# Kernel tuning notes

Hardware: AMD Instinct MI355X
Metric: run time of the kernel (lower is better)

Reference implementation:

```python
import jax, jax.numpy as jnp
import numpy as np

LN_EPS = 1e-5
LEAKY_SLOPE = 0.01  # torch nn.LeakyReLU default negative_slope


def layer_norm(x, gamma, beta):
    mu = jnp.mean(x, axis=-1, keepdims=True)
    var = jnp.mean(jnp.square(x - mu), axis=-1, keepdims=True)
    return (x - mu) * jax.lax.rsqrt(var + LN_EPS) * gamma + beta


def setup_inputs() -> dict:
    key = jax.random.key(0)
    k1, k2, k3 = jax.random.split(key, 3)
    B, N, D = 32, 128, 64
    embeddings = jax.random.normal(k1, (B, N, D), dtype=jnp.float32)
    ln_gamma = jnp.ones((D,), dtype=jnp.float32)
    ln_beta = jnp.zeros((D,), dtype=jnp.float32)
    # nn.Linear(3*D, 1): weight [1, 3D], bias [1]
    bound = 1.0 / np.sqrt(3 * D)
    att_w = jax.random.uniform(k2, (1, 3 * D), dtype=jnp.float32, minval=-bound, maxval=bound)
    att_b = jax.random.uniform(k3, (1,), dtype=jnp.float32, minval=-bound, maxval=bound)
    return {"embeddings": embeddings, "ln_gamma": ln_gamma, "ln_beta": ln_beta,
            "att_w": att_w, "att_b": att_b}


def reference(embeddings, ln_gamma, ln_beta, att_w, att_b):
    # embeddings: [B, N, D]
    D = embeddings.shape[-1]
    w = att_w[0]
    w_q, w_k, w_v = w[:D], w[D:2 * D], w[2 * D:]

    # value = query * key (all-pairs elementwise product), [B, N, N, D]
    value = embeddings[:, :, None, :] * embeddings[:, None, :, :]

    # LayerNorm of the broadcast query/key is just a per-node LayerNorm,
    # broadcast N-fold -> compute once per node, then contract with the
    # corresponding slice of the concat-linear weight.
    ln_e = layer_norm(embeddings, ln_gamma, ln_beta)           # [B, N, D]
    q_score = ln_e @ w_q                                        # [B, N]
    k_score = ln_e @ w_k                                        # [B, N]
    v_score = jnp.einsum('bijd,d->bij', layer_norm(value, ln_gamma, ln_beta), w_v)

    # score = Linear(concat(wq, wk, wv)) : [B, N, N]
    score = q_score[:, :, None] + k_score[:, None, :] + v_score + att_b[0]
    score = jnp.where(score >= 0, score, LEAKY_SLOPE * score)   # LeakyReLU
    # dropout is identity in eval mode
    alphas = jax.nn.softmax(score, axis=-1)[..., None]          # [B, N, N, 1]
    return (alphas, value)
```

## Files before the change

### kernel.cpp

```cpp
#include <hip/hip_runtime.h>

#define N_TOK 128
#define DIM   64
#define LN_EPS 1e-5f
#define SLOPE  0.01f

__device__ __forceinline__ float wave_reduce_sum(float v) {
#pragma unroll
    for (int off = 32; off >= 1; off >>= 1) v += __shfl_xor(v, off, 64);
    return v;
}
__device__ __forceinline__ float wave_reduce_max(float v) {
#pragma unroll
    for (int off = 32; off >= 1; off >>= 1) v = fmaxf(v, __shfl_xor(v, off, 64));
    return v;
}

__global__ __launch_bounds__(256) void k0_row_stats(
        const float* __restrict__ emb, const float* __restrict__ gamma,
        const float* __restrict__ beta, const float* __restrict__ attw,
        float* __restrict__ q_ws, float* __restrict__ k_ws, int nrows) {
    int wave = threadIdx.x >> 6, lane = threadIdx.x & 63;
    int r = blockIdx.x * 4 + wave;
    if (r >= nrows) return;
    float e  = emb[r * DIM + lane];
    float g  = gamma[lane], bt = beta[lane];
    float wq = attw[lane], wk = attw[DIM + lane];
    float gwq = g * wq, gwk = g * wk;

    float se  = wave_reduce_sum(e);
    float se2 = wave_reduce_sum(e * e);
    float sq  = wave_reduce_sum(e * gwq);
    float sk  = wave_reduce_sum(e * gwk);
    float Sgq = wave_reduce_sum(gwq);
    float Sbq = wave_reduce_sum(bt * wq);
    float Sgk = wave_reduce_sum(gwk);
    float Sbk = wave_reduce_sum(bt * wk);

    if (lane == 0) {
        float mu  = se * (1.f / 64.f);
        float var = se2 * (1.f / 64.f) - mu * mu;
        float rsq = rsqrtf(var + LN_EPS);
        q_ws[r] = rsq * (sq - mu * Sgq) + Sbq;
        k_ws[r] = rsq * (sk - mu * Sgk) + Sbk;
    }
}

__global__ __launch_bounds__(256) void k12_fused(
        const float* __restrict__ emb, const float* __restrict__ gamma,
        const float* __restrict__ beta, const float* __restrict__ attw,
        const float* __restrict__ attb, const float* __restrict__ q_ws,
        const float* __restrict__ k_ws, float* __restrict__ alphas,
        float4* __restrict__ value4) {
    __shared__ float sc_lds[N_TOK];

    int b = blockIdx.x >> 7;
    int i = blockIdx.x & 127;
    int c  = threadIdx.x & 15;
    int jg = threadIdx.x >> 4;

    const float4* E4 = (const float4*)emb + ((size_t)(b * N_TOK) << 4);
    float4 a4  = E4[(i << 4) | c];
    float4 g4  = ((const float4*)gamma)[c];
    float4 bt4 = ((const float4*)beta)[c];
    float4 wv4 = ((const float4*)(attw + 2 * DIM))[c];
    float gwx = g4.x * wv4.x, gwy = g4.y * wv4.y,
          gwz = g4.z * wv4.z, gww = g4.w * wv4.w;

    float Sg = gwx + gwy + gwz + gww;
    float Sb = bt4.x * wv4.x + bt4.y * wv4.y + bt4.z * wv4.z + bt4.w * wv4.w;
#pragma unroll
    for (int off = 1; off < 16; off <<= 1) {
        Sg += __shfl_xor(Sg, off);
        Sb += __shfl_xor(Sb, off);
    }
    float qi = q_ws[b * N_TOK + i] + attb[0];

    float4* vrow = value4 + ((size_t)blockIdx.x << 11);

#pragma unroll
    for (int it = 0; it < 8; ++it) {
        int j = (it << 4) | jg;
        float4 e4 = E4[(j << 4) | c];
        float4 t4;
        t4.x = a4.x * e4.x; t4.y = a4.y * e4.y;
        t4.z = a4.z * e4.z; t4.w = a4.w * e4.w;
        vrow[(j << 4) | c] = t4;

        float s1 = t4.x + t4.y + t4.z + t4.w;
        float s2 = t4.x * t4.x + t4.y * t4.y + t4.z * t4.z + t4.w * t4.w;
        float s3 = t4.x * gwx + t4.y * gwy + t4.z * gwz + t4.w * gww;
#pragma unroll
        for (int off = 1; off < 16; off <<= 1) {
            s1 += __shfl_xor(s1, off);
            s2 += __shfl_xor(s2, off);
            s3 += __shfl_xor(s3, off);
        }
        if (c == 0) {
            float mu  = s1 * (1.f / 64.f);
            float var = s2 * (1.f / 64.f) - mu * mu;
            float rsq = rsqrtf(var + LN_EPS);
            float vsc = rsq * (s3 - mu * Sg) + Sb;
            float sc  = qi + k_ws[b * N_TOK + j] + vsc;
            sc_lds[j] = sc >= 0.f ? sc : SLOPE * sc;
        }
    }
    __syncthreads();

    if (threadIdx.x < 64) {
        int lane = threadIdx.x;
        float va = sc_lds[lane];
        float vb = sc_lds[lane + 64];
        float m  = wave_reduce_max(fmaxf(va, vb));
        float ea = __expf(va - m), eb = __expf(vb - m);
        float s  = wave_reduce_sum(ea + eb);
        float inv = 1.f / s;
        float* arow = alphas + ((size_t)blockIdx.x << 7);
        arow[lane]      = ea * inv;
        arow[lane + 64] = eb * inv;
    }
}

extern "C" void kernel_launch(void* const* d_in, const int* in_sizes, int n_in,
                              void* d_out, int out_size, void* d_ws, size_t ws_size,
                              hipStream_t stream) {
    const float* emb   = (const float*)d_in[0];
    const float* gamma = (const float*)d_in[1];
    const float* beta  = (const float*)d_in[2];
    const float* attw  = (const float*)d_in[3];
    const float* attb  = (const float*)d_in[4];
    float* out = (float*)d_out;

    int B = in_sizes[0] / (N_TOK * DIM);
    int nrows = B * N_TOK;
    float* q_ws = (float*)d_ws;
    float* k_ws = q_ws + nrows;

    float* alphas = out;
    float* value  = out + (size_t)nrows * N_TOK;

    k0_row_stats<<<dim3((nrows + 3) / 4), dim3(256), 0, stream>>>(
        emb, gamma, beta, attw, q_ws, k_ws, nrows);
    k12_fused<<<dim3(nrows), dim3(256), 0, stream>>>(
        emb, gamma, beta, attw, attb, q_ws, k_ws, alphas, (float4*)value);
}
```

Before: 151.3 us.

## Use DPP row reductions, nontemporal value stores, defer LN epilogue to softmax wave

Replaces the 16-lane shuffle reductions with DPP row-sum operations and writes the large value tensor with nontemporal stores so it bypasses cache retention. The per-pair LayerNorm finishing math, the Sg/Sb reductions and the k_ws/q_ws loads move out of the hot loop into the single softmax wave, which works on partial sums staged in LDS. This is meant to shorten the loop and ease the store-bound write path, at the cost of more LDS traffic and a serialized epilogue in one wave. The DPP row_shr pattern leaves the complete sum only in lane 15 of each row, which is why that lane now does the LDS write.

```diff
diff --git a/kernel.cpp b/kernel.cpp
--- a/kernel.cpp
+++ b/kernel.cpp
@@ -4,6 +4,8 @@
 #define DIM   64
 #define LN_EPS 1e-5f
 #define SLOPE  0.01f
+
+typedef float f32x4 __attribute__((ext_vector_type(4)));
 
 __device__ __forceinline__ float wave_reduce_sum(float v) {
 #pragma unroll
@@ -13,6 +15,19 @@
 __device__ __forceinline__ float wave_reduce_max(float v) {
 #pragma unroll
     for (int off = 32; off >= 1; off >>= 1) v = fmaxf(v, __shfl_xor(v, off, 64));
+    return v;
+}
+
+template<int CTRL>
+__device__ __forceinline__ float dpp_add(float v) {
+    int p = __builtin_amdgcn_update_dpp(0, __float_as_int(v), CTRL, 0xF, 0xF, true);
+    return v + __int_as_float(p);
+}
+__device__ __forceinline__ float row16_sum(float v) {
+    v = dpp_add<0xB1>(v);
+    v = dpp_add<0x4E>(v);
+    v = dpp_add<0x114>(v);
+    v = dpp_add<0x118>(v);
     return v;
 }
 
@@ -51,73 +66,73 @@
         const float* __restrict__ beta, const float* __restrict__ attw,
         const float* __restrict__ attb, const float* __restrict__ q_ws,
         const float* __restrict__ k_ws, float* __restrict__ alphas,
-        float4* __restrict__ value4) {
-    __shared__ float sc_lds[N_TOK];
+        f32x4* __restrict__ value4) {
+    __shared__ float2 s12v[N_TOK];
+    __shared__ float  s3a[N_TOK];
 
     int b = blockIdx.x >> 7;
     int i = blockIdx.x & 127;
     int c  = threadIdx.x & 15;
     int jg = threadIdx.x >> 4;
 
-    const float4* E4 = (const float4*)emb + ((size_t)(b * N_TOK) << 4);
-    float4 a4  = E4[(i << 4) | c];
-    float4 g4  = ((const float4*)gamma)[c];
-    float4 bt4 = ((const float4*)beta)[c];
-    float4 wv4 = ((const float4*)(attw + 2 * DIM))[c];
-    float gwx = g4.x * wv4.x, gwy = g4.y * wv4.y,
-          gwz = g4.z * wv4.z, gww = g4.w * wv4.w;
+    const f32x4* E4 = (const f32x4*)emb + ((size_t)(b * N_TOK) << 4);
+    f32x4 a4  = E4[(i << 4) | c];
+    f32x4 g4  = ((const f32x4*)gamma)[c];
+    f32x4 wv4 = ((const f32x4*)(attw + 2 * DIM))[c];
+    f32x4 gw  = g4 * wv4;
 
-    float Sg = gwx + gwy + gwz + gww;
-    float Sb = bt4.x * wv4.x + bt4.y * wv4.y + bt4.z * wv4.z + bt4.w * wv4.w;
-#pragma unroll
-    for (int off = 1; off < 16; off <<= 1) {
-        Sg += __shfl_xor(Sg, off);
-        Sb += __shfl_xor(Sb, off);
-    }
-    float qi = q_ws[b * N_TOK + i] + attb[0];
-
-    float4* vrow = value4 + ((size_t)blockIdx.x << 11);
+    f32x4* vrow = value4 + ((size_t)blockIdx.x << 11);
 
 #pragma unroll
     for (int it = 0; it < 8; ++it) {
         int j = (it << 4) | jg;
-        float4 e4 = E4[(j << 4) | c];
-        float4 t4;
-        t4.x = a4.x * e4.x; t4.y = a4.y * e4.y;
-        t4.z = a4.z * e4.z; t4.w = a4.w * e4.w;
-        vrow[(j << 4) | c] = t4;
+        f32x4 e4 = E4[(j << 4) | c];
+        f32x4 t4 = a4 * e4;
+        __builtin_nontemporal_store(t4, &vrow[(j << 4) | c]);
 
-        float s1 = t4.x + t4.y + t4.z + t4.w;
-        float s2 = t4.x * t4.x + t4.y * t4.y + t4.z * t4.z + t4.w * t4.w;
-        float s3 = t4.x * gwx + t4.y * gwy + t4.z * gwz + t4.w * gww;
-#pragma unroll
-        for (int off = 1; off < 16; off <<= 1) {
-            s1 += __shfl_xor(s1, off);
-            s2 += __shfl_xor(s2, off);
-            s3 += __shfl_xor(s3, off);
-        }
-        if (c == 0) {
-            float mu  = s1 * (1.f / 64.f);
-            float var = s2 * (1.f / 64.f) - mu * mu;
-            float rsq = rsqrtf(var + LN_EPS);
-            float vsc = rsq * (s3 - mu * Sg) + Sb;
-            float sc  = qi + k_ws[b * N_TOK + j] + vsc;
-            sc_lds[j] = sc >= 0.f ? sc : SLOPE * sc;
+        float s1 = t4[0] + t4[1] + t4[2] + t4[3];
+        float s2 = t4[0]*t4[0] + t4[1]*t4[1] + t4[2]*t4[2] + t4[3]*t4[3];
+        float s3 = t4[0]*gw[0] + t4[1]*gw[1] + t4[2]*gw[2] + t4[3]*gw[3];
+        s1 = row16_sum(s1);
+        s2 = row16_sum(s2);
+        s3 = row16_sum(s3);
+        if (c == 15) {
+            s12v[j] = make_float2(s1, s2);
+            s3a[j]  = s3;
         }
     }
     __syncthreads();
 
     if (threadIdx.x < 64) {
         int lane = threadIdx.x;
-        float va = sc_lds[lane];
-        float vb = sc_lds[lane + 64];
-        float m  = wave_reduce_max(fmaxf(va, vb));
-        float ea = __expf(va - m), eb = __expf(vb - m);
-        float s  = wave_reduce_sum(ea + eb);
+        float g = gamma[lane], bt = beta[lane], wv = attw[2 * DIM + lane];
+        float Sg = wave_reduce_sum(g * wv);
+        float Sb = wave_reduce_sum(bt * wv);
+        float qi = q_ws[b * N_TOK + i] + attb[0];
+
+        float2 p0 = s12v[lane];
+        float2 p1 = s12v[lane + 64];
+        float s30 = s3a[lane], s31 = s3a[lane + 64];
+        float kj0 = k_ws[b * N_TOK + lane];
+        float kj1 = k_ws[b * N_TOK + lane + 64];
+
+        float mu0  = p0.x * (1.f / 64.f);
+        float var0 = p0.y * (1.f / 64.f) - mu0 * mu0;
+        float sc0  = qi + kj0 + rsqrtf(var0 + LN_EPS) * (s30 - mu0 * Sg) + Sb;
+        sc0 = sc0 >= 0.f ? sc0 : SLOPE * sc0;
+
+        float mu1  = p1.x * (1.f / 64.f);
+        float var1 = p1.y * (1.f / 64.f) - mu1 * mu1;
+        float sc1  = qi + kj1 + rsqrtf(var1 + LN_EPS) * (s31 - mu1 * Sg) + Sb;
+        sc1 = sc1 >= 0.f ? sc1 : SLOPE * sc1;
+
+        float m  = wave_reduce_max(fmaxf(sc0, sc1));
+        float e0 = __expf(sc0 - m), e1 = __expf(sc1 - m);
+        float s  = wave_reduce_sum(e0 + e1);
         float inv = 1.f / s;
         float* arow = alphas + ((size_t)blockIdx.x << 7);
-        arow[lane]      = ea * inv;
-        arow[lane + 64] = eb * inv;
+        arow[lane]      = e0 * inv;
+        arow[lane + 64] = e1 * inv;
     }
 }
 
@@ -142,5 +157,5 @@
     k0_row_stats<<<dim3((nrows + 3) / 4), dim3(256), 0, stream>>>(
         emb, gamma, beta, attw, q_ws, k_ws, nrows);
     k12_fused<<<dim3(nrows), dim3(256), 0, stream>>>(
-        emb, gamma, beta, attw, attb, q_ws, k_ws, alphas, (float4*)value);
+        emb, gamma, beta, attw, attb, q_ws, k_ws, alphas, (f32x4*)value);
 }
```

Result: slower. 157.4 us (+4.1%).
